# Optimization experiments

Hardware: AMD Instinct MI355X
Metric: run time of the kernel (lower is better)

The kernel has to match this reference:

```python
import jax, jax.numpy as jnp
import numpy as np

B, DIM, H, W = 2, 512, 48, 48
HEADS = 8
HD = DIM // HEADS
NS = 7
R = NS // 2
SCALE = HD ** -0.5
EPS = 1e-12


def _proj(x, w, b):
    # 1x1 conv == channel linear: x [B,C,H,W], w [O,C], b [O]
    return jnp.einsum('bchw,oc->bohw', x, w) + b[None, :, None, None]


def _to_heads(t):
    # [B,C,H,W] -> [B,heads,H,W,head_dim]
    return t.reshape(B, HEADS, HD, H, W).transpose(0, 1, 3, 4, 2)


def setup_inputs() -> dict:
    key = jax.random.key(0)
    ks = jax.random.split(key, 9)
    std = DIM ** -0.5
    inp = {'x': jax.random.normal(ks[0], (B, DIM, H, W), jnp.float32)}
    names = ['wq', 'bq', 'wk', 'bk', 'wv', 'bv', 'wo', 'bo']
    for i, n in enumerate(names):
        if n.startswith('w'):
            inp[n] = jax.random.normal(ks[i + 1], (DIM, DIM), jnp.float32) * std
        else:
            inp[n] = jnp.zeros((DIM,), jnp.float32)
    return inp


def reference(x, wq, bq, wk, bk, wv, bv, wo, bo):
    q = _proj(x, wq, bq)
    k = _proj(x, wk, bk)
    v = _proj(x, wv, bv)
    qh, kh, vh = _to_heads(q), _to_heads(k), _to_heads(v)

    offs = jnp.arange(-R, R + 1)
    oy, ox = jnp.meshgrid(offs, offs, indexing='ij')
    oy, ox = oy.reshape(-1), ox.reshape(-1)  # [K]
    by, bx = jnp.meshgrid(jnp.arange(H), jnp.arange(W), indexing='ij')
    ny = by[..., None] + oy  # [H,W,K]
    nx = bx[..., None] + ox
    valid = (ny >= 0) & (ny < H) & (nx >= 0) & (nx < W)  # [H,W,K]
    ny = jnp.clip(ny, 0, H - 1)
    nx = jnp.clip(nx, 0, W - 1)

    K = NS * NS
    T = H * W
    # gather neighborhoods: [B,heads,H,W,K,head_dim]
    k_nb = kh[:, :, ny, nx].reshape(B, HEADS, T, K, HD)
    v_nb = vh[:, :, ny, nx].reshape(B, HEADS, T, K, HD)
    q_tok = qh.reshape(B, HEADS, T, HD)

    scores = jnp.einsum('bhtd,bhtkd->bhtk', q_tok, k_nb) * SCALE
    neg = jnp.finfo(scores.dtype).min
    scores = jnp.where(valid.reshape(1, 1, T, K), scores, neg)
    attn = jax.nn.softmax(scores, axis=-1)
    out = jnp.einsum('bhtk,bhtkd->bhtd', attn, v_nb)

    # exclude self-value component (self-attention path)
    sv = vh.reshape(B, HEADS, T, HD)
    sv_unit = sv / jnp.maximum(jnp.linalg.norm(sv, axis=-1, keepdims=True), EPS)
    out = out - (out * sv_unit).sum(-1, keepdims=True) * sv_unit

    # [B,heads,T,HD] -> [B,C,H,W]
    out = out.reshape(B, HEADS, H, W, HD).transpose(0, 1, 4, 2, 3).reshape(B, DIM, H, W)
    return _proj(out, wo, bo)
```

## Files before the change

### kernel.cpp

```cpp
#include <hip/hip_runtime.h>
#include <hip/hip_bf16.h>
#include <math.h>

typedef __hip_bfloat16 bf16;
typedef __attribute__((ext_vector_type(4))) float f32x4;
typedef __attribute__((ext_vector_type(8))) short s16x8;
typedef __attribute__((ext_vector_type(4))) short s16x4;

#define B_     2
#define DIM_   512
#define Hh     48
#define Ww     48
#define T_     2304
#define HEADS_ 8
#define HD_    64
#define NS_    7
#define R_     3
#define KK_    49

typedef __attribute__((address_space(3))) unsigned       lds_u32_t;
typedef __attribute__((address_space(1))) const unsigned glb_u32_t;

__device__ __forceinline__ void gload16(const short* g, short* l) {
    __builtin_amdgcn_global_load_lds((glb_u32_t*)g, (lds_u32_t*)l, 16, 0, 0);
}

__device__ __forceinline__ short f2bs(float f) {
    bf16 h = __float2bfloat16(f);
    return *(short*)&h;
}

__device__ __forceinline__ float bs2f(short s) {
    bf16 h = *reinterpret_cast<const bf16*>(&s);
    return __bfloat162float(h);
}

__device__ __forceinline__ s16x8 cvt8(const float* __restrict__ p) {
    f32x4 a = *(const f32x4*)p;
    f32x4 b = *(const f32x4*)(p + 4);
    s16x8 r;
    r[0] = f2bs(a[0]); r[1] = f2bs(a[1]); r[2] = f2bs(a[2]); r[3] = f2bs(a[3]);
    r[4] = f2bs(b[0]); r[5] = f2bs(b[1]); r[6] = f2bs(b[2]); r[7] = f2bs(b[3]);
    return r;
}

__global__ __launch_bounds__(256) void prep(
    const float* __restrict__ x,
    const float* __restrict__ wq, const float* __restrict__ wk,
    const float* __restrict__ wv, const float* __restrict__ wo,
    bf16* __restrict__ xt, bf16* __restrict__ wb)
{
    __shared__ short tile[64 * 72];
    const int gid = blockIdx.x;
    const int tid = threadIdx.x;

    if (gid < 512) {
        const int i     = gid * 256 + tid;
        const int which = i >> 15;
        const int off   = (i & 32767) * 8;
        const float* src = (which == 0) ? wq : (which == 1) ? wk
                         : (which == 2) ? wv : wo;
        *(s16x8*)((short*)wb + which * 262144 + off) = cvt8(src + off);
        return;
    }

    const int pid = gid - 512;
    const int b   = pid / 288;
    const int rem = pid - b * 288;
    const int t0  = (rem % 36) * 64;
    const int c0  = (rem / 36) * 64;

    const float* X = x + (size_t)b * DIM_ * T_;

    const int c_l = tid >> 4;
    const int t4  = (tid & 15) * 4;
#pragma unroll
    for (int cp = 0; cp < 4; ++cp) {
        const int c = cp * 16 + c_l;
        f32x4 v = *(const f32x4*)(X + (size_t)(c0 + c) * T_ + t0 + t4);
#pragma unroll
        for (int e = 0; e < 4; ++e) tile[(t4 + e) * 72 + c] = f2bs(v[e]);
    }
    __syncthreads();

    const int t_l = tid >> 2;
    const int c16 = (tid & 3) * 16;
    short* dst = (short*)xt + ((size_t)b * T_ + t0 + t_l) * DIM_ + c0 + c16;
    *(s16x8*)(dst)     = *(const s16x8*)(&tile[t_l * 72 + c16]);
    *(s16x8*)(dst + 8) = *(const s16x8*)(&tile[t_l * 72 + c16 + 8]);
}

__global__ __launch_bounds__(256) void gemm_qkv(
    const bf16* __restrict__ xt, const bf16* __restrict__ wb,
    const float* __restrict__ bq, const float* __restrict__ bk,
    const float* __restrict__ bv,
    bf16* __restrict__ qb2, bf16* __restrict__ kb2, bf16* __restrict__ vb2)
{
    const int tt   = blockIdx.x * 128;
    const int ot   = blockIdx.y * 128;
    const int b    = blockIdx.z;
    const int proj = ot >> 9;
    const int orow = ot & 511;
    const int h0   = orow >> 6;

    const float* bsel = (proj == 0) ? bq : (proj == 1) ? bk : bv;
    const short* Wb   = (const short*)wb + proj * 262144;
    const short* X    = (const short*)xt + (size_t)b * T_ * DIM_;
    short*       sel  = (short*)((proj == 0) ? qb2 : (proj == 1) ? kb2 : vb2);

    __shared__ __align__(16) short Xs[128 * 32];
    __shared__ __align__(16) short Ws[128 * 32];

    const int tid  = threadIdx.x;
    const int lane = tid & 63;
    const int wid  = tid >> 6;
    const int ln   = lane & 15;
    const int qq   = lane >> 4;

    const int swz8 = (((lane & 3) ^ ((lane >> 3) & 3)) * 8);
    const int rsw  = (ln >> 1) & 3;

    f32x4 acc[2][8];
#pragma unroll
    for (int r = 0; r < 2; ++r)
#pragma unroll
        for (int n = 0; n < 8; ++n) acc[r][n] = (f32x4){0.f, 0.f, 0.f, 0.f};

    for (int kk = 0; kk < DIM_; kk += 32) {
#pragma unroll
        for (int half = 0; half < 2; ++half) {
            const int r0 = wid * 32 + half * 16;
            const int r  = r0 + (lane >> 2);
            gload16(X  + (size_t)(tt   + r) * DIM_ + kk + swz8, &Xs[r0 * 32]);
            gload16(Wb + (size_t)(orow + r) * DIM_ + kk + swz8, &Ws[r0 * 32]);
        }
        __syncthreads();

        s16x8 a[2];
#pragma unroll
        for (int r = 0; r < 2; ++r) {
            const int rr = r * 64 + wid * 16 + ln;
            a[r] = *(const s16x8*)&Xs[rr * 32 + ((qq ^ rsw) * 8)];
        }
#pragma unroll
        for (int n = 0; n < 8; ++n) {
            const int rw = n * 16 + ln;
            s16x8 bf = *(const s16x8*)&Ws[rw * 32 + ((qq ^ rsw) * 8)];
#pragma unroll
            for (int r = 0; r < 2; ++r)
                acc[r][n] = __builtin_amdgcn_mfma_f32_16x16x32_bf16(a[r], bf, acc[r][n], 0, 0, 0);
        }
        __syncthreads();
    }

    const size_t tb = (size_t)(b * HEADS_ + h0);
#pragma unroll
    for (int r = 0; r < 2; ++r)
#pragma unroll
        for (int n = 0; n < 8; ++n) {
            const int hn   = n >> 2;
            const int d    = (n & 3) * 16 + ln;
            const float bi = bsel[orow + n * 16 + ln];
#pragma unroll
            for (int e = 0; e < 4; ++e) {
                const int t = tt + r * 64 + wid * 16 + (lane >> 4) * 4 + e;
                sel[((tb + hn) * T_ + t) * HD_ + d] = f2bs(acc[r][n][e] + bi);
            }
        }
}

__global__ __launch_bounds__(256) void gemm_out(
    const bf16* __restrict__ ao, const bf16* __restrict__ wb,
    const float* __restrict__ bo, float* __restrict__ out)
{
    const int tt = blockIdx.x * 64;
    const int ot = blockIdx.y * 64;
    const int b  = blockIdx.z;

    const short* X  = (const short*)ao + (size_t)b * T_ * DIM_;
    const short* Wb = (const short*)wb + 3 * 262144;

    __shared__ __align__(16) short Ws[64 * 32];
    __shared__ __align__(16) short Xs[64 * 32];

    const int tid  = threadIdx.x;
    const int lane = tid & 63;
    const int wid  = tid >> 6;
    const int ln   = lane & 15;
    const int qq   = lane >> 4;

    const int swz8 = (((lane & 3) ^ ((lane >> 3) & 3)) * 8);
    const int rsw  = (ln >> 1) & 3;

    f32x4 acc[4];
#pragma unroll
    for (int n = 0; n < 4; ++n) acc[n] = (f32x4){0.f, 0.f, 0.f, 0.f};

    for (int kk = 0; kk < DIM_; kk += 32) {
        {
            const int r0 = wid * 16;
            const int r  = r0 + (lane >> 2);
            gload16(Wb + (size_t)(ot + r) * DIM_ + kk + swz8, &Ws[r0 * 32]);
            gload16(X  + (size_t)(tt + r) * DIM_ + kk + swz8, &Xs[r0 * 32]);
        }
        __syncthreads();

        s16x8 a = *(const s16x8*)&Ws[(wid * 16 + ln) * 32 + ((qq ^ rsw) * 8)];
#pragma unroll
        for (int n = 0; n < 4; ++n) {
            s16x8 bf = *(const s16x8*)&Xs[(n * 16 + ln) * 32 + ((qq ^ rsw) * 8)];
            acc[n] = __builtin_amdgcn_mfma_f32_16x16x32_bf16(a, bf, acc[n], 0, 0, 0);
        }
        __syncthreads();
    }

    float* obase = out + (size_t)b * DIM_ * T_;
#pragma unroll
    for (int n = 0; n < 4; ++n) {
        const int t = tt + n * 16 + ln;
#pragma unroll
        for (int e = 0; e < 4; ++e) {
            const int o    = ot + wid * 16 + (lane >> 4) * 4 + e;
            obase[(size_t)o * T_ + t] = acc[n][e] + bo[o];
        }
    }
}

__global__ __launch_bounds__(256, 4) void attn_mfma(
    const bf16* __restrict__ qb2, const bf16* __restrict__ kb2,
    const bf16* __restrict__ vb2, bf16* __restrict__ ao)
{
    __shared__ __align__(16) char smem[34048];
    short* Kl = (short*)smem;
    short* Ql = (short*)(smem + 25344);
    short* VT = (short*)smem;
    short* Pl = (short*)(smem + 27648);
    float* Ol = (float*)(smem + 27648);

    const int l   = blockIdx.x;
    const int idx = (l & 7) * 288 + (l >> 3);
    const int bh  = idx / 144;
    const int rem = idx - bh * 144;
    const int y   = rem / 3;
    const int x0  = (rem % 3) * 16;

    const short* qb  = (const short*)qb2 + (size_t)bh * T_ * HD_;
    const short* kb  = (const short*)kb2 + (size_t)bh * T_ * HD_;
    const short* vbb = (const short*)vb2 + (size_t)bh * T_ * HD_;

    const int tid  = threadIdx.x;
    const int lane = tid & 63;
    const int wv   = tid >> 6;
    const int qq   = lane >> 4;
    const int ln   = lane & 15;

    if (tid < 32) {
        const int t = tid >> 1, c = tid & 1;
        *(s16x8*)&Pl[t * 200 + 176 + c * 8] = (s16x8){0,0,0,0,0,0,0,0};
    }
    {
        const int c8 = (tid & 7) * 8;
        const int wr = tid >> 3;
#pragma unroll
        for (int p = 0; p < 6; ++p) {
            const int w = p * 32 + wr;
            if (w < 168) {
                const int wy = w / 24, u = w - wy * 24;
                if (u < 22) {
                    const int gy = min(max(y + wy - 3, 0), 47);
                    const int gx = min(max(x0 + u - 3, 0), 47);
                    *(s16x8*)&Kl[w * 72 + c8] =
                        *(const s16x8*)(kb + (size_t)(gy * 48 + gx) * 64 + c8);
                }
            }
        }
    }
    if (tid < 128) {
        const int t = tid >> 3, c8 = (tid & 7) * 8;
        *(s16x8*)&Ql[t * 72 + c8] =
            *(const s16x8*)(qb + (size_t)(y * 48 + x0 + t) * 64 + c8);
    }
    s16x4 vreg[10];
    {
        const int rr0 = tid >> 4;
        const int d4  = (tid & 15) * 4;
#pragma unroll
        for (int p = 0; p < 10; ++p) {
            const int rr = p * 16 + rr0;
            if (rr < 154) {
                const int wy = rr / 22, u = rr - wy * 22;
                const int gy = min(max(y + wy - 3, 0), 47);
                const int gx = min(max(x0 + u - 3, 0), 47);
                vreg[p] = *(const s16x4*)(vbb + (size_t)(gy * 48 + gx) * 64 + d4);
            }
        }
    }
    __syncthreads();

    f32x4 acc[11];
#pragma unroll
    for (int mt = 0; mt < 11; ++mt) acc[mt] = (f32x4){0.f, 0.f, 0.f, 0.f};
    __builtin_amdgcn_s_setprio(1);
#pragma unroll
    for (int ks = 0; ks < 2; ++ks) {
        s16x8 bq_ = *(const s16x8*)&Ql[ln * 72 + ks * 32 + qq * 8];
#pragma unroll
        for (int mt = 0; mt < 11; ++mt) {
            s16x8 ak = *(const s16x8*)&Kl[(mt * 16 + ln) * 72 + ks * 32 + qq * 8];
            acc[mt] = __builtin_amdgcn_mfma_f32_16x16x32_bf16(ak, bq_, acc[mt], 0, 0, 0);
        }
    }
    __builtin_amdgcn_s_setprio(0);

    const int dx = ln;
    float mxv = -3.0e38f;
#pragma unroll
    for (int mt = 0; mt < 11; ++mt) {
#pragma unroll
        for (int e = 0; e < 4; ++e) {
            const int w  = mt * 16 + qq * 4 + e;
            const int wy = w / 24, u = w - wy * 24;
            const bool valid = (w < 168) &&
                               ((unsigned)(u - dx) <= 6u) &&
                               ((unsigned)(y + wy - 3) < 48u) &&
                               ((unsigned)(x0 + u - 3) < 48u);
            const float s = valid ? acc[mt][e] * 0.125f : -3.0e38f;
            acc[mt][e] = s;
            mxv = fmaxf(mxv, s);
        }
    }
    mxv = fmaxf(mxv, __shfl_xor(mxv, 16));
    mxv = fmaxf(mxv, __shfl_xor(mxv, 32));
    float sum = 0.f;
#pragma unroll
    for (int mt = 0; mt < 11; ++mt)
#pragma unroll
        for (int e = 0; e < 4; ++e) {
            const float p = __expf(acc[mt][e] - mxv);
            acc[mt][e] = p;
            sum += p;
        }
    sum += __shfl_xor(sum, 16);
    sum += __shfl_xor(sum, 32);
    const float inv = 1.0f / sum;

#pragma unroll
    for (int mt = 0; mt < 11; ++mt) {
        const int owner = (mt >= 9) ? 3 : (mt / 3);
        if (wv == owner) {
#pragma unroll
            for (int e = 0; e < 4; ++e) {
                const int w = mt * 16 + qq * 4 + e;
                Pl[ln * 200 + w] = f2bs(acc[mt][e] * inv);
            }
        }
    }
    __syncthreads();

    {
        const int d = tid >> 2, c = tid & 3;
        *(s16x8*)&VT[d * 200 + 168 + c * 8] = (s16x8){0,0,0,0,0,0,0,0};
    }
#pragma unroll
    for (int pp = 0; pp < 2; ++pp) {
        const int r2 = pp * 256 + tid;
        if (r2 < 448) {
            const int wy = r2 >> 6, d = r2 & 63;
            *(unsigned*)&VT[d * 200 + wy * 24 + 22] = 0u;
        }
    }
    {
        const int rr0 = tid >> 4;
        const int d4  = (tid & 15) * 4;
        const int rot = tid & 3;
#pragma unroll
        for (int p = 0; p < 10; ++p) {
            const int rr = p * 16 + rr0;
            if (rr < 154) {
                const int wy = rr / 22, u = rr - wy * 22;
                const int w  = wy * 24 + u;
#pragma unroll
                for (int e = 0; e < 4; ++e) {
                    const int ee = (e + rot) & 3;
                    VT[(d4 + ee) * 200 + w] = vreg[p][ee];
                }
            }
        }
    }
    __syncthreads();

    f32x4 oacc = (f32x4){0.f, 0.f, 0.f, 0.f};
    __builtin_amdgcn_s_setprio(1);
#pragma unroll
    for (int ks = 0; ks < 6; ++ks) {
        s16x8 ap  = *(const s16x8*)&Pl[ln * 200 + ks * 32 + qq * 8];
        s16x8 bv_ = *(const s16x8*)&VT[(wv * 16 + ln) * 200 + ks * 32 + qq * 8];
        oacc = __builtin_amdgcn_mfma_f32_16x16x32_bf16(ap, bv_, oacc, 0, 0, 0);
    }
    __builtin_amdgcn_s_setprio(0);
    __syncthreads();
#pragma unroll
    for (int e = 0; e < 4; ++e)
        Ol[(qq * 4 + e) * 72 + wv * 16 + ln] = oacc[e];
    __syncthreads();

    {
        const int tt = tid >> 4;
        const int dl = tid & 15;
        const int tg = y * 48 + x0 + tt;
        const float o0 = Ol[tt * 72 + dl],      o1 = Ol[tt * 72 + dl + 16],
                    o2 = Ol[tt * 72 + dl + 32], o3 = Ol[tt * 72 + dl + 48];
        const short* vs = vbb + (size_t)tg * 64 + dl;
        const float v0 = bs2f(vs[0]),  v1 = bs2f(vs[16]),
                    v2 = bs2f(vs[32]), v3 = bs2f(vs[48]);
        float n2  = v0 * v0 + v1 * v1 + v2 * v2 + v3 * v3;
        float odv = o0 * v0 + o1 * v1 + o2 * v2 + o3 * v3;
#pragma unroll
        for (int off = 1; off < 16; off <<= 1) {
            n2  += __shfl_xor(n2, off);
            odv += __shfl_xor(odv, off);
        }
        const float mxn = fmaxf(sqrtf(n2), 1e-12f);
        const float cf  = odv / (mxn * mxn);
        const int b = bh >> 3, h = bh & 7;
        bf16* dst = ao + ((size_t)b * T_ + tg) * DIM_ + h * 64 + dl;
        dst[0]  = __float2bfloat16(o0 - cf * v0);
        dst[16] = __float2bfloat16(o1 - cf * v1);
        dst[32] = __float2bfloat16(o2 - cf * v2);
        dst[48] = __float2bfloat16(o3 - cf * v3);
    }
}

extern "C" void kernel_launch(void* const* d_in, const int* in_sizes, int n_in,
                              void* d_out, int out_size, void* d_ws, size_t ws_size,
                              hipStream_t stream)
{
    (void)in_sizes; (void)n_in; (void)out_size; (void)ws_size;

    const float* x  = (const float*)d_in[0];
    const float* wq = (const float*)d_in[1];
    const float* bq = (const float*)d_in[2];
    const float* wk = (const float*)d_in[3];
    const float* bk = (const float*)d_in[4];
    const float* wv = (const float*)d_in[5];
    const float* bv = (const float*)d_in[6];
    const float* wo = (const float*)d_in[7];
    const float* bo = (const float*)d_in[8];
    float* out = (float*)d_out;

    const size_t per = (size_t)B_ * HEADS_ * T_ * HD_;
    bf16* qb2 = (bf16*)d_ws;
    bf16* kb2 = qb2 + per;
    bf16* vb2 = kb2 + per;
    bf16* xa  = vb2 + per;
    bf16* wb  = xa + per;

    prep<<<dim3(512 + 576), 256, 0, stream>>>(x, wq, wk, wv, wo, xa, wb);

    dim3 g1(T_ / 128, 1536 / 128, B_);
    gemm_qkv<<<g1, 256, 0, stream>>>(xa, wb, bq, bk, bv, qb2, kb2, vb2);

    attn_mfma<<<dim3(B_ * HEADS_ * (T_ / 16)), 256, 0, stream>>>(qb2, kb2, vb2, xa);

    dim3 g2(T_ / 64, DIM_ / 64, B_);
    gemm_out<<<g2, 256, 0, stream>>>(xa, wb, bo, out);
}
```

Measured before the change: 62.49 us.

## Load K tile via direct global-to-LDS with XOR swizzle, keep Q in registers

The K neighborhood tile is now loaded with global_load_lds 16-byte direct copies into an unpadded 64-column LDS layout. An XOR swizzle on the source column replaces the padding for avoiding bank conflicts. Q fragments are loaded straight into registers instead of being staged through LDS, which shrinks shared memory. The aim is to cut register round-trips and LDS footprint in the prologue. In exchange, K rows are now loaded for all 168 window slots, including the unused padded columns.

```diff
diff --git a/kernel.cpp b/kernel.cpp
--- a/kernel.cpp
+++ b/kernel.cpp
@@ -230,12 +230,11 @@
     const bf16* __restrict__ qb2, const bf16* __restrict__ kb2,
     const bf16* __restrict__ vb2, bf16* __restrict__ ao)
 {
-    __shared__ __align__(16) char smem[34048];
+    __shared__ __align__(16) char smem[32000];
     short* Kl = (short*)smem;
-    short* Ql = (short*)(smem + 25344);
     short* VT = (short*)smem;
-    short* Pl = (short*)(smem + 27648);
-    float* Ol = (float*)(smem + 27648);
+    short* Pl = (short*)(smem + 25600);
+    float* Ol = (float*)(smem + 25600);
 
     const int l   = blockIdx.x;
     const int idx = (l & 7) * 288 + (l >> 3);
@@ -259,26 +258,24 @@
         *(s16x8*)&Pl[t * 200 + 176 + c * 8] = (s16x8){0,0,0,0,0,0,0,0};
     }
     {
-        const int c8 = (tid & 7) * 8;
-        const int wr = tid >> 3;
+        const int swc = (((lane & 7) ^ (lane >> 3)) & 7) * 8;
 #pragma unroll
         for (int p = 0; p < 6; ++p) {
-            const int w = p * 32 + wr;
-            if (w < 168) {
-                const int wy = w / 24, u = w - wy * 24;
-                if (u < 22) {
-                    const int gy = min(max(y + wy - 3, 0), 47);
-                    const int gx = min(max(x0 + u - 3, 0), 47);
-                    *(s16x8*)&Kl[w * 72 + c8] =
-                        *(const s16x8*)(kb + (size_t)(gy * 48 + gx) * 64 + c8);
-                }
+            const int g = p * 4 + wv;
+            if (g < 21) {
+                const int r  = g * 8 + (lane >> 3);
+                const int wy = r / 24, u = r - wy * 24;
+                const int gy = min(max(y + wy - 3, 0), 47);
+                const int gx = min(max(x0 + u - 3, 0), 47);
+                gload16(kb + (size_t)(gy * 48 + gx) * 64 + swc, &Kl[g * 8 * 64]);
             }
         }
     }
-    if (tid < 128) {
-        const int t = tid >> 3, c8 = (tid & 7) * 8;
-        *(s16x8*)&Ql[t * 72 + c8] =
-            *(const s16x8*)(qb + (size_t)(y * 48 + x0 + t) * 64 + c8);
+    s16x8 qreg0, qreg1;
+    {
+        const short* qp = qb + (size_t)(y * 48 + x0 + ln) * 64 + qq * 8;
+        qreg0 = *(const s16x8*)(qp);
+        qreg1 = *(const s16x8*)(qp + 32);
     }
     s16x4 vreg[10];
     {
@@ -303,10 +300,11 @@
     __builtin_amdgcn_s_setprio(1);
 #pragma unroll
     for (int ks = 0; ks < 2; ++ks) {
-        s16x8 bq_ = *(const s16x8*)&Ql[ln * 72 + ks * 32 + qq * 8];
+        s16x8 bq_ = (ks == 0) ? qreg0 : qreg1;
 #pragma unroll
         for (int mt = 0; mt < 11; ++mt) {
-            s16x8 ak = *(const s16x8*)&Kl[(mt * 16 + ln) * 72 + ks * 32 + qq * 8];
+            const int rr = mt * 16 + ln;
+            s16x8 ak = *(const s16x8*)&Kl[rr * 64 + (((ks * 4 + qq) ^ (ln & 7)) * 8)];
             acc[mt] = __builtin_amdgcn_mfma_f32_16x16x32_bf16(ak, bq_, acc[mt], 0, 0, 0);
         }
     }
```

Result: faster. 59.64 us (median of 2 runs) (-4.5%).
